# Kernel tuning notes

Hardware: AMD Instinct MI355X
Metric: run time of the kernel (lower is better)

The kernel has to match this reference:

```python
import jax, jax.numpy as jnp
import numpy as np

N_USERS = 200_000
N_ITEMS = 100_000
N_NODES = N_USERS + N_ITEMS
EMB = 100          # emb_size; transForm1 in_features=200 == 2*EMB
NNZ = 1_000_000    # raw user-item interactions
BATCH = 16_384
N_LAYERS = 4


def _build_norm_adj(rng):
    """Replicates get_norm_adj_mat: symmetric bipartite adjacency + self-loops,
    D^-0.5 A D^-0.5 normalization. Returns COO (row, col, vals)."""
    uid = rng.integers(0, N_USERS, NNZ).astype(np.int64)
    iid = rng.integers(0, N_ITEMS, NNZ).astype(np.int64) + N_USERS
    # dok_matrix dict-update dedupes repeated (u,i) pairs
    pair_key = uid * N_NODES + iid
    _, keep = np.unique(pair_key, return_index=True)
    uid, iid = uid[keep], iid[keep]
    loops = np.arange(N_NODES, dtype=np.int64)
    row = np.concatenate([uid, iid, loops])
    col = np.concatenate([iid, uid, loops])
    deg = np.bincount(row, minlength=N_NODES).astype(np.float32)  # (A>0) row sums
    dinv = deg ** -0.5
    vals = dinv[row] * dinv[col]
    return row.astype(np.int32), col.astype(np.int32), vals.astype(np.float32)


def setup_inputs() -> dict:
    key = jax.random.key(0)
    ks = jax.random.split(key, 16)
    rng = np.random.default_rng(0)
    adj_row, adj_col, adj_vals = _build_norm_adj(rng)

    def lin(k, fan_in, fan_out):
        # torch Linear default init: U(-1/sqrt(fan_in), 1/sqrt(fan_in))
        bound = 1.0 / np.sqrt(fan_in)
        kw, kb = jax.random.split(k)
        W = jax.random.uniform(kw, (fan_in, fan_out), jnp.float32, -bound, bound)
        b = jax.random.uniform(kb, (fan_out,), jnp.float32, -bound, bound)
        return W, b

    W1, b1 = lin(ks[0], 200, 128)
    W4, b4 = lin(ks[1], 128, 64)
    W2, b2 = lin(ks[2], 64, 32)
    W3, b3 = lin(ks[3], 32, 1)

    return {
        "userIdx": jax.random.randint(ks[4], (BATCH,), 0, N_USERS, jnp.int32),
        "itemIdx": jax.random.randint(ks[5], (BATCH,), 0, N_ITEMS, jnp.int32),
        "adj_row": jnp.asarray(adj_row),
        "adj_col": jnp.asarray(adj_col),
        "adj_vals": jnp.asarray(adj_vals),
        "user_emb": jax.random.normal(ks[6], (N_USERS, EMB), jnp.float32),
        "item_emb": jax.random.normal(ks[7], (N_ITEMS, EMB), jnp.float32),
        "W1": W1, "b1": b1, "W4": W4, "b4": b4,
        "W2": W2, "b2": b2, "W3": W3, "b3": b3,
        "u_bias": jax.random.normal(ks[8], (N_USERS, 1), jnp.float32),
        "i_bias": jax.random.normal(ks[9], (N_USERS + N_ITEMS, 1), jnp.float32),
    }


def reference(userIdx, itemIdx, adj_row, adj_col, adj_vals,
              user_emb, item_emb, W1, b1, W4, b4, W2, b2, W3, b3,
              u_bias, i_bias):
    item_nodes = itemIdx + N_USERS
    # LightGCN propagation: 4 sparse SpMM layers, mean over {0..4} embeddings
    emb = jnp.concatenate([user_emb, item_emb], axis=0)   # [N_NODES, EMB]
    acc = emb
    x = emb
    for _ in range(N_LAYERS):
        x = jax.ops.segment_sum(adj_vals[:, None] * x[adj_col], adj_row,
                                num_segments=N_NODES)
        acc = acc + x
    final = acc / float(N_LAYERS + 1)

    u = final[userIdx]          # [B, EMB]
    i = final[item_nodes]       # [B, EMB]
    h = jnp.concatenate([u, i], axis=1)          # [B, 200]
    h = jax.nn.relu(h @ W1 + b1)                 # transForm1 + ReLU
    h = h @ W4 + b4                              # transForm4
    h = h @ W2 + b2                              # transForm2
    h = h @ W3 + b3                              # transForm3 -> [B, 1]
    bias = u_bias[userIdx, 0] + i_bias[item_nodes, 0]
    return h.ravel() + bias
```

## Files before the change

kernel.cpp:

```cpp
#include <hip/hip_runtime.h>
#include <hip/hip_bf16.h>

#define N_USERS 200000
#define N_ITEMS 100000
#define N_NODES 300000
#define EMB 100
#define XSTRIDE 64
#define BATCH 16384
#define UNR 8

#define SCAN_BLK 1024
#define NBLK ((N_NODES + SCAN_BLK - 1) / SCAN_BLK)

__device__ __forceinline__ unsigned int f2bf(float f) {
    unsigned int x = __float_as_uint(f);
    return (x + 0x7fffu + ((x >> 16) & 1u)) >> 16;
}
__device__ __forceinline__ float bf_lo(unsigned int u) { return __uint_as_float(u << 16); }
__device__ __forceinline__ float bf_hi(unsigned int u) { return __uint_as_float(u & 0xffff0000u); }


__global__ void hist_kernel(const int* __restrict__ row, int* __restrict__ cnt, int n) {
    for (int i = blockIdx.x * blockDim.x + threadIdx.x; i < n; i += gridDim.x * blockDim.x)
        atomicAdd(&cnt[row[i]], 1);
}

__global__ __launch_bounds__(SCAN_BLK) void block_reduce_kernel(const int* __restrict__ cnt,
                                                                int* __restrict__ bsum, int n) {
    __shared__ int sm[SCAN_BLK];
    int i = blockIdx.x * SCAN_BLK + threadIdx.x;
    sm[threadIdx.x] = (i < n) ? cnt[i] : 0;
    __syncthreads();
    for (int off = SCAN_BLK / 2; off > 0; off >>= 1) {
        if (threadIdx.x < off) sm[threadIdx.x] += sm[threadIdx.x + off];
        __syncthreads();
    }
    if (threadIdx.x == 0) bsum[blockIdx.x] = sm[0];
}

__global__ __launch_bounds__(512) void scan_bsum_kernel(int* __restrict__ bsum,
                                                        int* __restrict__ rp_total) {
    __shared__ int sm[512];
    int v = (threadIdx.x < NBLK) ? bsum[threadIdx.x] : 0;
    sm[threadIdx.x] = v;
    __syncthreads();
    for (int off = 1; off < 512; off <<= 1) {
        int t = (threadIdx.x >= off) ? sm[threadIdx.x - off] : 0;
        __syncthreads();
        sm[threadIdx.x] += t;
        __syncthreads();
    }
    if (threadIdx.x < NBLK) bsum[threadIdx.x] = sm[threadIdx.x] - v;
    if (threadIdx.x == 511) rp_total[0] = sm[511];
}

__global__ __launch_bounds__(SCAN_BLK) void block_scan_kernel(const int* __restrict__ cnt,
                                                              const int* __restrict__ bsum,
                                                              int* __restrict__ rp, int n) {
    __shared__ int sm[SCAN_BLK];
    int i = blockIdx.x * SCAN_BLK + threadIdx.x;
    int v = (i < n) ? cnt[i] : 0;
    sm[threadIdx.x] = v;
    __syncthreads();
    for (int off = 1; off < SCAN_BLK; off <<= 1) {
        int t = (threadIdx.x >= off) ? sm[threadIdx.x - off] : 0;
        __syncthreads();
        sm[threadIdx.x] += t;
        __syncthreads();
    }
    if (i < n) rp[i] = bsum[blockIdx.x] + sm[threadIdx.x] - v;
}

__global__ void copy_user_kernel(const int* __restrict__ col, const float* __restrict__ val,
                                 int2* __restrict__ cedge, int Eu) {
    for (int i = blockIdx.x * blockDim.x + threadIdx.x; i < Eu; i += gridDim.x * blockDim.x)
        cedge[i] = make_int2(col[i], __float_as_int(val[i]));
}

__global__ void scatter_item_kernel(const int* __restrict__ row, const int* __restrict__ col,
                                    const float* __restrict__ val, int* __restrict__ cur,
                                    int2* __restrict__ cedge, int Eu) {
    for (int i = blockIdx.x * blockDim.x + threadIdx.x; i < Eu; i += gridDim.x * blockDim.x) {
        int ii = Eu + i;
        int r = row[ii];
        int p = atomicAdd(&cur[r], 1);
        cedge[p] = make_int2(col[ii], __float_as_int(val[ii]));
    }
}


__global__ __launch_bounds__(256) void conv_kernel(const float* __restrict__ user_emb,
                                                   const float* __restrict__ item_emb,
                                                   unsigned int* __restrict__ x) {
    int node = blockIdx.x * 4 + (threadIdx.x >> 6);
    int lane = threadIdx.x & 63;
    unsigned int u = 0;
    if (lane < 50) {
        const float* src = (node < N_USERS) ? (user_emb + (size_t)node * EMB)
                                            : (item_emb + (size_t)(node - N_USERS) * EMB);
        float2 v = ((const float2*)src)[lane];
        u = f2bf(v.x) | (f2bf(v.y) << 16);
    }
    x[(size_t)node * XSTRIDE + lane] = u;
}


__global__ __launch_bounds__(256) void spmm_kernel(const int* __restrict__ rp,
                                                   const int2* __restrict__ cedge,
                                                   const float* __restrict__ vloop,
                                                   const unsigned int* __restrict__ xin,
                                                   unsigned int* __restrict__ xout) {
    int row = blockIdx.x * 4 + (threadIdx.x >> 6);
    int lane = threadIdx.x & 63;
    int s = rp[row], e = rp[row + 1];
    float vl = vloop[row];
    unsigned int urow = xin[(size_t)row * XSTRIDE + lane];
    float ax = vl * bf_lo(urow), ay = vl * bf_hi(urow);
    if (s < e) {
        for (int j0 = s; j0 < e; j0 += UNR) {
            int2 ed[UNR];
            #pragma unroll
            for (int k = 0; k < UNR; ++k) {
                int j = j0 + k; if (j > e - 1) j = e - 1;
                ed[k] = cedge[j];
            }
            unsigned int u[UNR];
            #pragma unroll
            for (int k = 0; k < UNR; ++k)
                u[k] = xin[(size_t)ed[k].x * XSTRIDE + lane];
            #pragma unroll
            for (int k = 0; k < UNR; ++k) {
                float v = (j0 + k < e) ? __int_as_float(ed[k].y) : 0.f;
                ax += v * bf_lo(u[k]);
                ay += v * bf_hi(u[k]);
            }
        }
    }
    xout[(size_t)row * XSTRIDE + lane] = f2bf(ax) | (f2bf(ay) << 16);
}


__global__ __launch_bounds__(256) void batch_spmm_kernel(const int* __restrict__ rp,
        const int2* __restrict__ cedge, const float* __restrict__ vloop,
        const unsigned int* __restrict__ xin,
        const int* __restrict__ uidx, const int* __restrict__ iidx,
        float* __restrict__ acc) {
    int t = blockIdx.x * 4 + (threadIdx.x >> 6);
    int lane = threadIdx.x & 63;
    int b = t >> 1, half = t & 1;
    int row = half ? (iidx[b] + N_USERS) : uidx[b];
    int s = rp[row], e = rp[row + 1];
    float vl = vloop[row];
    unsigned int urow = xin[(size_t)row * XSTRIDE + lane];
    float ax = vl * bf_lo(urow), ay = vl * bf_hi(urow);
    if (s < e) {
        for (int j0 = s; j0 < e; j0 += UNR) {
            int2 ed[UNR];
            #pragma unroll
            for (int k = 0; k < UNR; ++k) {
                int j = j0 + k; if (j > e - 1) j = e - 1;
                ed[k] = cedge[j];
            }
            unsigned int u[UNR];
            #pragma unroll
            for (int k = 0; k < UNR; ++k)
                u[k] = xin[(size_t)ed[k].x * XSTRIDE + lane];
            #pragma unroll
            for (int k = 0; k < UNR; ++k) {
                float v = (j0 + k < e) ? __int_as_float(ed[k].y) : 0.f;
                ax += v * bf_lo(u[k]);
                ay += v * bf_hi(u[k]);
            }
        }
    }
    if (lane < 50) {
        float2* arow = (float2*)(acc + (size_t)b * 200 + half * 100);
        float2 old = arow[lane];
        arow[lane] = make_float2(old.x + ax, old.y + ay);
    }
}


__global__ __launch_bounds__(256) void gather_init_kernel(const float* __restrict__ user_emb,
                                                          const float* __restrict__ item_emb,
                                                          const int* __restrict__ uidx,
                                                          const int* __restrict__ iidx,
                                                          float* __restrict__ acc) {
    int b = blockIdx.x * 4 + (threadIdx.x >> 6);
    int lane = threadIdx.x & 63;
    if (lane >= 50) return;
    const float2* ur = (const float2*)(user_emb + (size_t)uidx[b] * EMB);
    const float2* ir = (const float2*)(item_emb + (size_t)iidx[b] * EMB);
    float2* a2 = (float2*)(acc + (size_t)b * 200);
    a2[lane] = ur[lane];
    a2[50 + lane] = ir[lane];
}

__global__ __launch_bounds__(256) void gather_kernel(const unsigned int* __restrict__ x,
                                                     const int* __restrict__ uidx,
                                                     const int* __restrict__ iidx,
                                                     float* __restrict__ acc) {
    int b = blockIdx.x * 4 + (threadIdx.x >> 6);
    int lane = threadIdx.x & 63;
    if (lane >= 50) return;
    unsigned int uu = x[(size_t)uidx[b] * XSTRIDE + lane];
    unsigned int iu = x[(size_t)(iidx[b] + N_USERS) * XSTRIDE + lane];
    float2* a2 = (float2*)(acc + (size_t)b * 200);
    float2 o0 = a2[lane], o1 = a2[50 + lane];
    a2[lane] = make_float2(o0.x + bf_lo(uu), o0.y + bf_hi(uu));
    a2[50 + lane] = make_float2(o1.x + bf_lo(iu), o1.y + bf_hi(iu));
}


__global__ __launch_bounds__(512) void mlp_kernel(const float* __restrict__ acc,
        const float* __restrict__ W1, const float* __restrict__ b1,
        const float* __restrict__ W4, const float* __restrict__ b4,
        const float* __restrict__ W2, const float* __restrict__ b2,
        const float* __restrict__ W3, const float* __restrict__ b3,
        const int* __restrict__ uidx, const int* __restrict__ iidx,
        const float* __restrict__ u_bias, const float* __restrict__ i_bias,
        float* __restrict__ out) {
    __shared__ float W1s[200 * 128];
    __shared__ float in_s[8][2][200];
    __shared__ float h1_s[8][2][128];
    __shared__ float h2_s[8][2][64];
    int tid = threadIdx.x;
    for (int i = tid; i < 200 * 128 / 4; i += 512)
        ((float4*)W1s)[i] = ((const float4*)W1)[i];
    __syncthreads();

    int w = tid >> 6, lane = tid & 63;
    int row0 = blockIdx.x * 64 + w * 8;
    for (int pr = 0; pr < 4; ++pr) {
        int ba = row0 + pr * 2, bb = ba + 1;
        for (int t = lane; t < 200; t += 64) {
            in_s[w][0][t] = acc[(size_t)ba * 200 + t] * 0.2f;
            in_s[w][1][t] = acc[(size_t)bb * 200 + t] * 0.2f;
        }
        {
            float s0a = b1[lane], s1a = b1[64 + lane];
            float s0b = s0a, s1b = s1a;
            for (int k = 0; k < 200; ++k) {
                float wa = W1s[k * 128 + lane], wb = W1s[k * 128 + 64 + lane];
                float ia = in_s[w][0][k], ib = in_s[w][1][k];
                s0a += ia * wa; s1a += ia * wb;
                s0b += ib * wa; s1b += ib * wb;
            }
            h1_s[w][0][lane] = fmaxf(s0a, 0.f);
            h1_s[w][0][64 + lane] = fmaxf(s1a, 0.f);
            h1_s[w][1][lane] = fmaxf(s0b, 0.f);
            h1_s[w][1][64 + lane] = fmaxf(s1b, 0.f);
        }
        __syncthreads();
        {
            float sa = b4[lane], sb = sa;
            for (int k = 0; k < 128; ++k) {
                float wv = W4[k * 64 + lane];
                sa += h1_s[w][0][k] * wv;
                sb += h1_s[w][1][k] * wv;
            }
            h2_s[w][0][lane] = sa;
            h2_s[w][1][lane] = sb;
        }
        float pa = 0.f, pb = 0.f;
        if (lane < 32) {
            float sa = b2[lane], sb = sa;
            for (int k = 0; k < 64; ++k) {
                float wv = W2[k * 32 + lane];
                sa += h2_s[w][0][k] * wv;
                sb += h2_s[w][1][k] * wv;
            }
            float w3 = W3[lane];
            pa = sa * w3;
            pb = sb * w3;
        }
        #pragma unroll
        for (int off = 16; off >= 1; off >>= 1) {
            pa += __shfl_xor(pa, off);
            pb += __shfl_xor(pb, off);
        }
        if (lane == 0) {
            out[ba] = pa + b3[0] + u_bias[uidx[ba]] + i_bias[iidx[ba] + N_USERS];
            out[bb] = pb + b3[0] + u_bias[uidx[bb]] + i_bias[iidx[bb] + N_USERS];
        }
    }
}


extern "C" void kernel_launch(void* const* d_in, const int* in_sizes, int n_in,
                              void* d_out, int out_size, void* d_ws, size_t ws_size,
                              hipStream_t stream) {
    const int*   userIdx  = (const int*)d_in[0];
    const int*   itemIdx  = (const int*)d_in[1];
    const int*   adj_row  = (const int*)d_in[2];
    const int*   adj_col  = (const int*)d_in[3];
    const float* adj_vals = (const float*)d_in[4];
    const float* user_emb = (const float*)d_in[5];
    const float* item_emb = (const float*)d_in[6];
    const float* W1 = (const float*)d_in[7],  *b1 = (const float*)d_in[8];
    const float* W4 = (const float*)d_in[9],  *b4 = (const float*)d_in[10];
    const float* W2 = (const float*)d_in[11], *b2 = (const float*)d_in[12];
    const float* W3 = (const float*)d_in[13], *b3 = (const float*)d_in[14];
    const float* u_bias = (const float*)d_in[15];
    const float* i_bias = (const float*)d_in[16];
    const int E = in_sizes[2];
    const int Eu = (E - N_NODES) / 2;
    const float* vloop = adj_vals + (size_t)2 * Eu;

    char* ws = (char*)d_ws;
    size_t off = 0;
    auto carve = [&](size_t bytes) -> char* {
        char* p = ws + off;
        off += (bytes + 255) & ~(size_t)255;
        return p;
    };
    int*   rp    = (int*)  carve((size_t)(N_NODES + 1) * sizeof(int));
    int*   cur   = (int*)  carve((size_t)N_NODES * sizeof(int));
    int*   bsum  = (int*)  carve((size_t)NBLK * sizeof(int));
    int2*  cedge = (int2*) carve((size_t)2 * Eu * sizeof(int2));
    unsigned int* x0 = (unsigned int*)carve((size_t)N_NODES * XSTRIDE * 4);
    unsigned int* x1 = (unsigned int*)carve((size_t)N_NODES * XSTRIDE * 4);
    float* accb  = (float*)carve((size_t)BATCH * 2 * EMB * sizeof(float));
    (void)ws_size; (void)n_in; (void)out_size;

    hipMemsetAsync(cur, 0, (size_t)N_NODES * sizeof(int), stream);
    hist_kernel<<<2048, 256, 0, stream>>>(adj_row, cur, 2 * Eu);
    block_reduce_kernel<<<NBLK, SCAN_BLK, 0, stream>>>(cur, bsum, N_NODES);
    scan_bsum_kernel<<<1, 512, 0, stream>>>(bsum, rp + N_NODES);
    block_scan_kernel<<<NBLK, SCAN_BLK, 0, stream>>>(cur, bsum, rp, N_NODES);
    hipMemcpyAsync(cur + N_USERS, rp + N_USERS, (size_t)N_ITEMS * sizeof(int),
                   hipMemcpyDeviceToDevice, stream);
    copy_user_kernel<<<2048, 256, 0, stream>>>(adj_col, adj_vals, cedge, Eu);
    scatter_item_kernel<<<2048, 256, 0, stream>>>(adj_row, adj_col, adj_vals, cur, cedge, Eu);

    conv_kernel<<<N_NODES / 4, 256, 0, stream>>>(user_emb, item_emb, x0);

    gather_init_kernel<<<BATCH / 4, 256, 0, stream>>>(user_emb, item_emb, userIdx, itemIdx, accb);

    spmm_kernel<<<N_NODES / 4, 256, 0, stream>>>(rp, cedge, vloop, x0, x1);
    gather_kernel<<<BATCH / 4, 256, 0, stream>>>(x1, userIdx, itemIdx, accb);
    spmm_kernel<<<N_NODES / 4, 256, 0, stream>>>(rp, cedge, vloop, x1, x0);
    gather_kernel<<<BATCH / 4, 256, 0, stream>>>(x0, userIdx, itemIdx, accb);
    spmm_kernel<<<N_NODES / 4, 256, 0, stream>>>(rp, cedge, vloop, x0, x1);
    gather_kernel<<<BATCH / 4, 256, 0, stream>>>(x1, userIdx, itemIdx, accb);

    batch_spmm_kernel<<<2 * BATCH / 4, 256, 0, stream>>>(rp, cedge, vloop, x1,
                                                         userIdx, itemIdx, accb);

    mlp_kernel<<<BATCH / 64, 512, 0, stream>>>(accb, W1, b1, W4, b4, W2, b2, W3, b3,
                                               userIdx, itemIdx, u_bias, i_bias,
                                               (float*)d_out);
}
```

Baseline: 859.1 us.

## Fuse gather passes into SpMM launches and merge CSR build kernels

The per-layer batch gather kernels become extra rider blocks on the SpMM and conversion launches. The final layer's gather is folded into batch_spmm by adding 1 to the self-loop weight. CSR construction merges the histogram with the user-edge copy, and the scan with the cursor init, which drops a kernel and a device-to-device memcpy. Smaller tweaks add readfirstlane on row indices, 32-bit index arithmetic, a simpler unrolled edge loop and removal of a block barrier in the MLP. The aim is to cut launch overhead and tail gaps between small kernels, at the cost of mixing heterogeneous work inside one grid.

```diff
diff --git a/kernel.cpp b/kernel.cpp
--- a/kernel.cpp
+++ b/kernel.cpp
@@ -8,6 +8,8 @@
 #define XSTRIDE 64
 #define BATCH 16384
 #define UNR 8
+#define NROWBLK (N_NODES / 4)
+#define NRIDER (BATCH / 4)
 
 #define SCAN_BLK 1024
 #define NBLK ((N_NODES + SCAN_BLK - 1) / SCAN_BLK)
@@ -20,9 +22,14 @@
 __device__ __forceinline__ float bf_hi(unsigned int u) { return __uint_as_float(u & 0xffff0000u); }
 
 
-__global__ void hist_kernel(const int* __restrict__ row, int* __restrict__ cnt, int n) {
-    for (int i = blockIdx.x * blockDim.x + threadIdx.x; i < n; i += gridDim.x * blockDim.x)
+__global__ void hist_copy_kernel(const int* __restrict__ row, const int* __restrict__ col,
+                                 const float* __restrict__ val, int* __restrict__ cnt,
+                                 int2* __restrict__ cedge, int Eu) {
+    for (int i = blockIdx.x * blockDim.x + threadIdx.x; i < 2 * Eu;
+         i += gridDim.x * blockDim.x) {
         atomicAdd(&cnt[row[i]], 1);
+        if (i < Eu) cedge[i] = make_int2(col[i], __float_as_int(val[i]));
+    }
 }
 
 __global__ __launch_bounds__(SCAN_BLK) void block_reduce_kernel(const int* __restrict__ cnt,
@@ -56,7 +63,8 @@
 
 __global__ __launch_bounds__(SCAN_BLK) void block_scan_kernel(const int* __restrict__ cnt,
                                                               const int* __restrict__ bsum,
-                                                              int* __restrict__ rp, int n) {
+                                                              int* __restrict__ rp,
+                                                              int* __restrict__ cur, int n) {
     __shared__ int sm[SCAN_BLK];
     int i = blockIdx.x * SCAN_BLK + threadIdx.x;
     int v = (i < n) ? cnt[i] : 0;
@@ -68,13 +76,11 @@
         sm[threadIdx.x] += t;
         __syncthreads();
     }
-    if (i < n) rp[i] = bsum[blockIdx.x] + sm[threadIdx.x] - v;
-}
-
-__global__ void copy_user_kernel(const int* __restrict__ col, const float* __restrict__ val,
-                                 int2* __restrict__ cedge, int Eu) {
-    for (int i = blockIdx.x * blockDim.x + threadIdx.x; i < Eu; i += gridDim.x * blockDim.x)
-        cedge[i] = make_int2(col[i], __float_as_int(val[i]));
+    if (i < n) {
+        int x = bsum[blockIdx.x] + sm[threadIdx.x] - v;
+        rp[i] = x;
+        if (i >= N_USERS) cur[i] = x;
+    }
 }
 
 __global__ void scatter_item_kernel(const int* __restrict__ row, const int* __restrict__ col,
@@ -91,17 +97,31 @@
 
 __global__ __launch_bounds__(256) void conv_kernel(const float* __restrict__ user_emb,
                                                    const float* __restrict__ item_emb,
-                                                   unsigned int* __restrict__ x) {
-    int node = blockIdx.x * 4 + (threadIdx.x >> 6);
-    int lane = threadIdx.x & 63;
+                                                   unsigned int* __restrict__ x,
+                                                   const int* __restrict__ uidx,
+                                                   const int* __restrict__ iidx,
+                                                   float* __restrict__ acc) {
+    int bid = blockIdx.x;
+    int wv = threadIdx.x >> 6, lane = threadIdx.x & 63;
+    if (bid >= NROWBLK) {
+        int b = (bid - NROWBLK) * 4 + wv;
+        if (lane >= 50) return;
+        const float2* ur = (const float2*)(user_emb + (unsigned)uidx[b] * EMB);
+        const float2* ir = (const float2*)(item_emb + (unsigned)iidx[b] * EMB);
+        float2* a2 = (float2*)(acc + (unsigned)b * 200);
+        a2[lane] = ur[lane];
+        a2[50 + lane] = ir[lane];
+        return;
+    }
+    int node = bid * 4 + wv;
     unsigned int u = 0;
     if (lane < 50) {
-        const float* src = (node < N_USERS) ? (user_emb + (size_t)node * EMB)
-                                            : (item_emb + (size_t)(node - N_USERS) * EMB);
+        const float* src = (node < N_USERS) ? (user_emb + (unsigned)node * EMB)
+                                            : (item_emb + (unsigned)(node - N_USERS) * EMB);
         float2 v = ((const float2*)src)[lane];
         u = f2bf(v.x) | (f2bf(v.y) << 16);
     }
-    x[(size_t)node * XSTRIDE + lane] = u;
+    x[((unsigned)node << 6) + lane] = u;
 }
 
 
@@ -109,34 +129,46 @@
                                                    const int2* __restrict__ cedge,
                                                    const float* __restrict__ vloop,
                                                    const unsigned int* __restrict__ xin,
-                                                   unsigned int* __restrict__ xout) {
-    int row = blockIdx.x * 4 + (threadIdx.x >> 6);
-    int lane = threadIdx.x & 63;
+                                                   unsigned int* __restrict__ xout,
+                                                   const int* __restrict__ uidx,
+                                                   const int* __restrict__ iidx,
+                                                   float* __restrict__ acc) {
+    int bid = blockIdx.x;
+    int wv = threadIdx.x >> 6, lane = threadIdx.x & 63;
+    if (bid >= NROWBLK) {
+        int b = (bid - NROWBLK) * 4 + wv;
+        if (lane >= 50) return;
+        unsigned int uu = xin[((unsigned)uidx[b] << 6) + lane];
+        unsigned int iu = xin[(((unsigned)iidx[b] + N_USERS) << 6) + lane];
+        float2* a2 = (float2*)(acc + (unsigned)b * 200);
+        float2 o0 = a2[lane], o1 = a2[50 + lane];
+        a2[lane] = make_float2(o0.x + bf_lo(uu), o0.y + bf_hi(uu));
+        a2[50 + lane] = make_float2(o1.x + bf_lo(iu), o1.y + bf_hi(iu));
+        return;
+    }
+    int row = __builtin_amdgcn_readfirstlane(bid * 4 + wv);
     int s = rp[row], e = rp[row + 1];
     float vl = vloop[row];
-    unsigned int urow = xin[(size_t)row * XSTRIDE + lane];
+    unsigned int urow = xin[((unsigned)row << 6) + lane];
     float ax = vl * bf_lo(urow), ay = vl * bf_hi(urow);
-    if (s < e) {
-        for (int j0 = s; j0 < e; j0 += UNR) {
-            int2 ed[UNR];
-            #pragma unroll
-            for (int k = 0; k < UNR; ++k) {
-                int j = j0 + k; if (j > e - 1) j = e - 1;
-                ed[k] = cedge[j];
-            }
-            unsigned int u[UNR];
-            #pragma unroll
-            for (int k = 0; k < UNR; ++k)
-                u[k] = xin[(size_t)ed[k].x * XSTRIDE + lane];
-            #pragma unroll
-            for (int k = 0; k < UNR; ++k) {
-                float v = (j0 + k < e) ? __int_as_float(ed[k].y) : 0.f;
-                ax += v * bf_lo(u[k]);
-                ay += v * bf_hi(u[k]);
-            }
-        }
-    }
-    xout[(size_t)row * XSTRIDE + lane] = f2bf(ax) | (f2bf(ay) << 16);
+    for (int j0 = s; j0 < e; j0 += UNR) {
+        int n = e - j0;
+        int2 ed[UNR];
+        #pragma unroll
+        for (int k = 0; k < UNR; ++k)
+            ed[k] = cedge[j0 + ((k < n) ? k : 0)];
+        unsigned int u[UNR];
+        #pragma unroll
+        for (int k = 0; k < UNR; ++k)
+            u[k] = xin[((unsigned)ed[k].x << 6) + lane];
+        #pragma unroll
+        for (int k = 0; k < UNR; ++k) {
+            float v = (k < n) ? __int_as_float(ed[k].y) : 0.f;
+            ax += v * bf_lo(u[k]);
+            ay += v * bf_hi(u[k]);
+        }
+    }
+    xout[((unsigned)row << 6) + lane] = f2bf(ax) | (f2bf(ay) << 16);
 }
 
 
@@ -148,67 +180,33 @@
     int t = blockIdx.x * 4 + (threadIdx.x >> 6);
     int lane = threadIdx.x & 63;
     int b = t >> 1, half = t & 1;
-    int row = half ? (iidx[b] + N_USERS) : uidx[b];
+    int row = __builtin_amdgcn_readfirstlane(half ? (iidx[b] + N_USERS) : uidx[b]);
     int s = rp[row], e = rp[row + 1];
-    float vl = vloop[row];
-    unsigned int urow = xin[(size_t)row * XSTRIDE + lane];
+    float vl = vloop[row] + 1.0f;
+    unsigned int urow = xin[((unsigned)row << 6) + lane];
     float ax = vl * bf_lo(urow), ay = vl * bf_hi(urow);
-    if (s < e) {
-        for (int j0 = s; j0 < e; j0 += UNR) {
-            int2 ed[UNR];
-            #pragma unroll
-            for (int k = 0; k < UNR; ++k) {
-                int j = j0 + k; if (j > e - 1) j = e - 1;
-                ed[k] = cedge[j];
-            }
-            unsigned int u[UNR];
-            #pragma unroll
-            for (int k = 0; k < UNR; ++k)
-                u[k] = xin[(size_t)ed[k].x * XSTRIDE + lane];
-            #pragma unroll
-            for (int k = 0; k < UNR; ++k) {
-                float v = (j0 + k < e) ? __int_as_float(ed[k].y) : 0.f;
-                ax += v * bf_lo(u[k]);
-                ay += v * bf_hi(u[k]);
-            }
+    for (int j0 = s; j0 < e; j0 += UNR) {
+        int n = e - j0;
+        int2 ed[UNR];
+        #pragma unroll
+        for (int k = 0; k < UNR; ++k)
+            ed[k] = cedge[j0 + ((k < n) ? k : 0)];
+        unsigned int u[UNR];
+        #pragma unroll
+        for (int k = 0; k < UNR; ++k)
+            u[k] = xin[((unsigned)ed[k].x << 6) + lane];
+        #pragma unroll
+        for (int k = 0; k < UNR; ++k) {
+            float v = (k < n) ? __int_as_float(ed[k].y) : 0.f;
+            ax += v * bf_lo(u[k]);
+            ay += v * bf_hi(u[k]);
         }
     }
     if (lane < 50) {
-        float2* arow = (float2*)(acc + (size_t)b * 200 + half * 100);
+        float2* arow = (float2*)(acc + (unsigned)b * 200 + half * 100);
         float2 old = arow[lane];
         arow[lane] = make_float2(old.x + ax, old.y + ay);
     }
-}
-
-
-__global__ __launch_bounds__(256) void gather_init_kernel(const float* __restrict__ user_emb,
-                                                          const float* __restrict__ item_emb,
-                                                          const int* __restrict__ uidx,
-                                                          const int* __restrict__ iidx,
-                                                          float* __restrict__ acc) {
-    int b = blockIdx.x * 4 + (threadIdx.x >> 6);
-    int lane = threadIdx.x & 63;
-    if (lane >= 50) return;
-    const float2* ur = (const float2*)(user_emb + (size_t)uidx[b] * EMB);
-    const float2* ir = (const float2*)(item_emb + (size_t)iidx[b] * EMB);
-    float2* a2 = (float2*)(acc + (size_t)b * 200);
-    a2[lane] = ur[lane];
-    a2[50 + lane] = ir[lane];
-}
-
-__global__ __launch_bounds__(256) void gather_kernel(const unsigned int* __restrict__ x,
-                                                     const int* __restrict__ uidx,
-                                                     const int* __restrict__ iidx,
-                                                     float* __restrict__ acc) {
-    int b = blockIdx.x * 4 + (threadIdx.x >> 6);
-    int lane = threadIdx.x & 63;
-    if (lane >= 50) return;
-    unsigned int uu = x[(size_t)uidx[b] * XSTRIDE + lane];
-    unsigned int iu = x[(size_t)(iidx[b] + N_USERS) * XSTRIDE + lane];
-    float2* a2 = (float2*)(acc + (size_t)b * 200);
-    float2 o0 = a2[lane], o1 = a2[50 + lane];
-    a2[lane] = make_float2(o0.x + bf_lo(uu), o0.y + bf_hi(uu));
-    a2[50 + lane] = make_float2(o1.x + bf_lo(iu), o1.y + bf_hi(iu));
 }
 
 
@@ -234,8 +232,8 @@
     for (int pr = 0; pr < 4; ++pr) {
         int ba = row0 + pr * 2, bb = ba + 1;
         for (int t = lane; t < 200; t += 64) {
-            in_s[w][0][t] = acc[(size_t)ba * 200 + t] * 0.2f;
-            in_s[w][1][t] = acc[(size_t)bb * 200 + t] * 0.2f;
+            in_s[w][0][t] = acc[(unsigned)ba * 200 + t] * 0.2f;
+            in_s[w][1][t] = acc[(unsigned)bb * 200 + t] * 0.2f;
         }
         {
             float s0a = b1[lane], s1a = b1[64 + lane];
@@ -251,7 +249,6 @@
             h1_s[w][1][lane] = fmaxf(s0b, 0.f);
             h1_s[w][1][64 + lane] = fmaxf(s1b, 0.f);
         }
-        __syncthreads();
         {
             float sa = b4[lane], sb = sa;
             for (int k = 0; k < 128; ++k) {
@@ -324,25 +321,21 @@
     (void)ws_size; (void)n_in; (void)out_size;
 
     hipMemsetAsync(cur, 0, (size_t)N_NODES * sizeof(int), stream);
-    hist_kernel<<<2048, 256, 0, stream>>>(adj_row, cur, 2 * Eu);
+    hist_copy_kernel<<<2048, 256, 0, stream>>>(adj_row, adj_col, adj_vals, cur, cedge, Eu);
     block_reduce_kernel<<<NBLK, SCAN_BLK, 0, stream>>>(cur, bsum, N_NODES);
     scan_bsum_kernel<<<1, 512, 0, stream>>>(bsum, rp + N_NODES);
-    block_scan_kernel<<<NBLK, SCAN_BLK, 0, stream>>>(cur, bsum, rp, N_NODES);
-    hipMemcpyAsync(cur + N_USERS, rp + N_USERS, (size_t)N_ITEMS * sizeof(int),
-                   hipMemcpyDeviceToDevice, stream);
-    copy_user_kernel<<<2048, 256, 0, stream>>>(adj_col, adj_vals, cedge, Eu);
+    block_scan_kernel<<<NBLK, SCAN_BLK, 0, stream>>>(cur, bsum, rp, cur, N_NODES);
     scatter_item_kernel<<<2048, 256, 0, stream>>>(adj_row, adj_col, adj_vals, cur, cedge, Eu);
 
-    conv_kernel<<<N_NODES / 4, 256, 0, stream>>>(user_emb, item_emb, x0);
-
-    gather_init_kernel<<<BATCH / 4, 256, 0, stream>>>(user_emb, item_emb, userIdx, itemIdx, accb);
-
-    spmm_kernel<<<N_NODES / 4, 256, 0, stream>>>(rp, cedge, vloop, x0, x1);
-    gather_kernel<<<BATCH / 4, 256, 0, stream>>>(x1, userIdx, itemIdx, accb);
-    spmm_kernel<<<N_NODES / 4, 256, 0, stream>>>(rp, cedge, vloop, x1, x0);
-    gather_kernel<<<BATCH / 4, 256, 0, stream>>>(x0, userIdx, itemIdx, accb);
-    spmm_kernel<<<N_NODES / 4, 256, 0, stream>>>(rp, cedge, vloop, x0, x1);
-    gather_kernel<<<BATCH / 4, 256, 0, stream>>>(x1, userIdx, itemIdx, accb);
+    conv_kernel<<<NROWBLK + NRIDER, 256, 0, stream>>>(user_emb, item_emb, x0,
+                                                      userIdx, itemIdx, accb);
+
+    spmm_kernel<<<NROWBLK, 256, 0, stream>>>(rp, cedge, vloop, x0, x1,
+                                             userIdx, itemIdx, accb);
+    spmm_kernel<<<NROWBLK + NRIDER, 256, 0, stream>>>(rp, cedge, vloop, x1, x0,
+                                                      userIdx, itemIdx, accb);
+    spmm_kernel<<<NROWBLK + NRIDER, 256, 0, stream>>>(rp, cedge, vloop, x0, x1,
+                                                      userIdx, itemIdx, accb);
 
     batch_spmm_kernel<<<2 * BATCH / 4, 256, 0, stream>>>(rp, cedge, vloop, x1,
                                                          userIdx, itemIdx, accb);
```

Measured after the change: 737.4 us. 1.16x faster.
